# Kernel tuning notes

Measured on AMD Instinct MI355X. Metric: run time of the kernel, lower is better.

Reference implementation:

```python
import jax, jax.numpy as jnp
import numpy as np

DIM = 1024
NUM_HEADS = 16
HEAD_DIM = DIM // NUM_HEADS
SCALE = HEAD_DIM ** -0.5


def setup_inputs() -> dict:
    key = jax.random.key(0)
    k_x, k_qkv, k_pw, k_pb = jax.random.split(key, 4)
    B, S = 2, 2048
    x = jax.random.normal(k_x, (B, S, DIM), dtype=jnp.float32)
    # nn.Linear(dim, 3*dim, bias=False): weight [3*dim, dim]
    w_qkv = jax.random.normal(k_qkv, (3 * DIM, DIM), dtype=jnp.float32) * (DIM ** -0.5)
    # nn.Linear(dim, dim): weight [dim, dim], bias [dim]
    w_proj = jax.random.normal(k_pw, (DIM, DIM), dtype=jnp.float32) * (DIM ** -0.5)
    b_proj = jax.random.normal(k_pb, (DIM,), dtype=jnp.float32) * 0.01
    return {"x": x, "w_qkv": w_qkv, "w_proj": w_proj, "b_proj": b_proj}


def reference(x, w_qkv, w_proj, b_proj):
    B, S, D = x.shape
    qkv = jnp.einsum("bsd,ed->bse", x, w_qkv)  # [B,S,3D]
    q, k, v = jnp.split(qkv, 3, axis=-1)
    def heads(t):  # [B,S,D] -> [B,H,S,hd]
        return t.reshape(B, S, NUM_HEADS, HEAD_DIM).transpose(0, 2, 1, 3)
    q, k, v = heads(q), heads(k), heads(v)
    attn = jnp.einsum("bhqd,bhkd->bhqk", q, k) * SCALE  # [B,H,S,S]
    attn = jax.nn.softmax(attn, axis=-1)
    out = jnp.einsum("bhqk,bhkd->bhqd", attn, v)  # [B,H,S,hd]
    out = out.transpose(0, 2, 1, 3).reshape(B, S, D)
    return jnp.einsum("bsd,ed->bse", out, w_proj) + b_proj
```

## Files before the change

kernel.cpp:

```cpp
#include <hip/hip_runtime.h>
#include <stdint.h>

typedef __bf16 bf16;
typedef __bf16 bf16x8 __attribute__((ext_vector_type(8)));
typedef float f32x4 __attribute__((ext_vector_type(4)));
typedef float f32x16 __attribute__((ext_vector_type(16)));

typedef __attribute__((address_space(1))) void gvoid_t;
typedef __attribute__((address_space(3))) void lvoid_t;

__device__ __forceinline__ void gload16(const void* src, void* lds) {
    __builtin_amdgcn_global_load_lds((gvoid_t*)src, (lvoid_t*)lds, 16, 0, 0);
}

__device__ __forceinline__ float fexp2(float x) {
    float r;
    asm("v_exp_f32 %0, %1" : "=v"(r) : "v"(x));
    return r;
}

__global__ __launch_bounds__(256) void cvt3_kernel(const float* __restrict__ x,
                                                   const float* __restrict__ wqkv,
                                                   const float* __restrict__ wproj,
                                                   bf16* __restrict__ xb,
                                                   bf16* __restrict__ wqkvb,
                                                   bf16* __restrict__ wprojb) {
    int idx = blockIdx.x * 256 + threadIdx.x;
    int stride = gridDim.x * 256;
    for (int i = idx; i < 1048576; i += stride) {
        const float* in;
        bf16* out;
        int j;
        if (i < 524288) { in = x; out = xb; j = i; }
        else if (i < 917504) { in = wqkv; out = wqkvb; j = i - 524288; }
        else { in = wproj; out = wprojb; j = i - 917504; }
        const float4* p = (const float4*)in;
        float4 a = p[(long)j * 2], b = p[(long)j * 2 + 1];
        bf16x8 o;
        o[0] = (bf16)a.x; o[1] = (bf16)a.y; o[2] = (bf16)a.z; o[3] = (bf16)a.w;
        o[4] = (bf16)b.x; o[5] = (bf16)b.y; o[6] = (bf16)b.z; o[7] = (bf16)b.w;
        ((bf16x8*)out)[j] = o;
    }
}

template <bool F32OUT, int BN>
__global__ __launch_bounds__(256) void gemm_bt(const bf16* __restrict__ A,
                                               const bf16* __restrict__ W,
                                               const float* __restrict__ bias,
                                               void* __restrict__ Cout,
                                               const int M, const int N, const int K) {
    constexpr int NT = BN / 32;
    constexpr int BELEMS = BN * 32;
    __shared__ __align__(16) bf16 Alds[3 * 4096];
    __shared__ __align__(16) bf16 Blds[3 * BELEMS];
    const int t = threadIdx.x;
    const int wid = t >> 6, lane = t & 63;
    const int g = lane >> 4, c = lane & 15;
    const int wm = wid >> 1, wn = wid & 1;
    const long bm = (long)blockIdx.y * 128, bn = (long)blockIdx.x * BN;

    f32x4 acc[4][NT] = {};

    const int arow = t >> 2;
    const int acol = (t & 3) * 8;
    const bf16* Asrc = A + (bm + arow) * (long)K + acol;
    const bf16* Bsrc = W + (bn + arow) * (long)K + acol;
    const int dstb = wid * 512;

#define GSTAGE(BI)                                                       \
    {                                                                    \
        bf16* ad = Alds + (BI) * 4096 + dstb;                            \
        bf16* bd = Blds + (BI) * BELEMS + dstb;                          \
        gload16(Asrc, ad);                                               \
        gload16(Asrc + (long)64 * K, ad + 2048);                         \
        gload16(Bsrc, bd);                                               \
        if constexpr (BN == 128) gload16(Bsrc + (long)64 * K, bd + 2048);\
        Asrc += 32;                                                      \
        Bsrc += 32;                                                      \
    }

    auto computeg = [&](int bi) __attribute__((always_inline)) {
        const bf16* Ab = Alds + bi * 4096;
        const bf16* Bb = Blds + bi * BELEMS;
        bf16x8 af[4], bfr[NT];
#pragma unroll
        for (int mt = 0; mt < 4; ++mt)
            af[mt] = *(const bf16x8*)(Ab + (wm * 64 + mt * 16 + c) * 32 + g * 8);
#pragma unroll
        for (int nt = 0; nt < NT; ++nt)
            bfr[nt] = *(const bf16x8*)(Bb + (wn * (BN / 2) + nt * 16 + c) * 32 + g * 8);
#pragma unroll
        for (int mt = 0; mt < 4; ++mt)
#pragma unroll
            for (int nt = 0; nt < NT; ++nt)
                acc[mt][nt] = __builtin_amdgcn_mfma_f32_16x16x32_bf16(af[mt], bfr[nt],
                                                                      acc[mt][nt], 0, 0, 0);
    };

#define GWAITN                                                              \
    if constexpr (BN == 128) { asm volatile("s_waitcnt vmcnt(4)" ::: "memory"); } \
    else { asm volatile("s_waitcnt vmcnt(3)" ::: "memory"); }

#define GSTEP(CUR, NXT)            \
    GWAITN;                        \
    __builtin_amdgcn_s_barrier();  \
    GSTAGE(NXT);                   \
    computeg(CUR);

    GSTAGE(0);
    GSTAGE(1);
    for (int t3 = 0; t3 < 10; ++t3) {
        GSTEP(0, 2)
        GSTEP(1, 0)
        GSTEP(2, 1)
    }
    GWAITN;
    __builtin_amdgcn_s_barrier();
    computeg(0);
    asm volatile("s_waitcnt vmcnt(0)" ::: "memory");
    __builtin_amdgcn_s_barrier();
    computeg(1);
#undef GSTEP
#undef GWAITN
#undef GSTAGE

#pragma unroll
    for (int mt = 0; mt < 4; ++mt) {
#pragma unroll
        for (int nt = 0; nt < NT; ++nt) {
#pragma unroll
            for (int i = 0; i < 4; ++i) {
                const long row = bm + wm * 64 + mt * 16 + g * 4 + i;
                const long col = bn + wn * (BN / 2) + nt * 16 + c;
                if constexpr (F32OUT) {
                    ((float*)Cout)[row * N + col] = acc[mt][nt][i] + bias[col];
                } else {
                    ((bf16*)Cout)[row * N + col] = (bf16)acc[mt][nt][i];
                }
            }
        }
    }
}

__global__ __launch_bounds__(128) void flash_kernel(const bf16* __restrict__ qk,
                                                    const bf16* __restrict__ Vt,
                                                    bf16* __restrict__ attno) {
    __shared__ __align__(16) bf16 KV[24576];
    __shared__ float LP[128];

    const int t = threadIdx.x;
    const int wid = t >> 6, lane = t & 63;
    const int l31 = lane & 31, hl = lane >> 5;

    const int i0 = blockIdx.x;
    const int xcd = i0 & 7, slot = i0 >> 3;
    const int bh = xcd * 4 + (slot >> 4);
    const int qb = slot & 15;
    const int b = bh >> 4, h = bh & 15;
    const int rowbase = b * 2048;
    const int q0w = qb * 128 + wid * 64;

    bf16x8 qfa[4], qfb[4];
    {
        const bf16* qra = qk + (long)(rowbase + q0w + l31) * 2048 + h * 64 + hl * 8;
        const bf16* qrb = qra + 32 * 2048;
        const float qs = 0.18033688f;
#pragma unroll
        for (int ks = 0; ks < 4; ++ks) {
            bf16x8 a = *(const bf16x8*)(qra + ks * 16);
            bf16x8 d = *(const bf16x8*)(qrb + ks * 16);
#pragma unroll
            for (int e = 0; e < 8; ++e) {
                qfa[ks][e] = (bf16)((float)a[e] * qs);
                qfb[ks][e] = (bf16)((float)d[e] * qs);
            }
        }
    }

    const int srow0 = wid * 8 + ((lane >> 3) & 7);
    const int swcol = ((lane & 7) ^ (srow0 & 7)) * 8;
    const bf16* ksn = qk + (long)(rowbase + srow0) * 2048 + 1024 + h * 64 + swcol;
    const bf16* vsn = Vt + (long)(h * 64 + srow0) * 4096 + b * 2048 + swcol;
    const int kchunk = wid * 512;

    int rdoff[4];
#pragma unroll
    for (int ks = 0; ks < 4; ++ks)
        rdoff[ks] = l31 * 64 + (((ks * 2 + hl) ^ (l31 & 7)) * 8);

    float lpA0 = 0.f, lpB0 = 0.f, lpA1 = 0.f, lpB1 = 0.f;
    f32x16 oacc00 = {}, oacc10 = {}, oacc01 = {}, oacc11 = {};

#define STAGE(BI)                                                        \
    {                                                                    \
        bf16* kd = KV + (BI) * 4096 + kchunk;                            \
        bf16* vd = KV + 12288 + (BI) * 4096 + kchunk;                    \
        gload16(ksn, kd);                                                \
        gload16(ksn + 32768, kd + 1024);                                 \
        gload16(ksn + 65536, kd + 2048);                                 \
        gload16(ksn + 98304, kd + 3072);                                 \
        gload16(vsn, vd);                                                \
        gload16(vsn + 65536, vd + 1024);                                 \
        gload16(vsn + 131072, vd + 2048);                                \
        gload16(vsn + 196608, vd + 3072);                                \
        ksn += 131072;                                                   \
        vsn += 64;                                                       \
    }

    auto compute = [&](int bi) __attribute__((always_inline)) {
        const bf16* Kb = KV + bi * 4096;
        const bf16* Vb = KV + 12288 + bi * 4096;
        f32x16 s00 = {}, s10 = {}, s01 = {}, s11 = {};
        __builtin_amdgcn_s_setprio(1);
#pragma unroll
        for (int ks = 0; ks < 4; ++ks) {
            bf16x8 kf0 = *(const bf16x8*)(Kb + rdoff[ks]);
            bf16x8 kf1 = *(const bf16x8*)(Kb + 2048 + rdoff[ks]);
            s00 = __builtin_amdgcn_mfma_f32_32x32x16_bf16(kf0, qfa[ks], s00, 0, 0, 0);
            s10 = __builtin_amdgcn_mfma_f32_32x32x16_bf16(kf1, qfa[ks], s10, 0, 0, 0);
            s01 = __builtin_amdgcn_mfma_f32_32x32x16_bf16(kf0, qfb[ks], s01, 0, 0, 0);
            s11 = __builtin_amdgcn_mfma_f32_32x32x16_bf16(kf1, qfb[ks], s11, 0, 0, 0);
        }
        __builtin_amdgcn_s_setprio(0);
        float p00[16], p10[16], p01[16], p11[16];
#pragma unroll
        for (int r = 0; r < 16; ++r) p00[r] = fexp2(s00[r]);
#pragma unroll
        for (int r = 0; r < 16; ++r) p10[r] = fexp2(s10[r]);
#pragma unroll
        for (int r = 0; r < 16; ++r) p01[r] = fexp2(s01[r]);
#pragma unroll
        for (int r = 0; r < 16; ++r) p11[r] = fexp2(s11[r]);
#pragma unroll
        for (int r = 0; r < 8; ++r) {
            lpA0 += p00[r] + p10[r];
            lpB0 += p00[r + 8] + p10[r + 8];
            lpA1 += p01[r] + p11[r];
            lpB1 += p01[r + 8] + p11[r + 8];
        }
        __builtin_amdgcn_s_setprio(1);
#pragma unroll
        for (int ks = 0; ks < 4; ++ks) {
            bf16x8 vf0 = *(const bf16x8*)(Vb + rdoff[ks]);
            bf16x8 vf1 = *(const bf16x8*)(Vb + 2048 + rdoff[ks]);
            const int s = (ks & 1) * 8;
            {
                const float* pp = (ks < 2) ? p00 : p10;
                unsigned wA, wB, wC, wD;
                asm("v_cvt_pk_bf16_f32 %0, %1, %2" : "=v"(wA) : "v"(pp[s + 0]), "v"(pp[s + 1]));
                asm("v_cvt_pk_bf16_f32 %0, %1, %2" : "=v"(wB) : "v"(pp[s + 4]), "v"(pp[s + 5]));
                asm("v_cvt_pk_bf16_f32 %0, %1, %2" : "=v"(wC) : "v"(pp[s + 2]), "v"(pp[s + 3]));
                asm("v_cvt_pk_bf16_f32 %0, %1, %2" : "=v"(wD) : "v"(pp[s + 6]), "v"(pp[s + 7]));
                asm("v_permlane32_swap_b32 %0, %1" : "+v"(wA), "+v"(wB));
                asm("v_permlane32_swap_b32 %0, %1" : "+v"(wC), "+v"(wD));
                union { unsigned w[4]; bf16x8 v; } pu;
                pu.w[0] = wA; pu.w[1] = wC; pu.w[2] = wB; pu.w[3] = wD;
                oacc00 = __builtin_amdgcn_mfma_f32_32x32x16_bf16(pu.v, vf0, oacc00, 0, 0, 0);
                oacc10 = __builtin_amdgcn_mfma_f32_32x32x16_bf16(pu.v, vf1, oacc10, 0, 0, 0);
            }
            {
                const float* pp = (ks < 2) ? p01 : p11;
                unsigned wA, wB, wC, wD;
                asm("v_cvt_pk_bf16_f32 %0, %1, %2" : "=v"(wA) : "v"(pp[s + 0]), "v"(pp[s + 1]));
                asm("v_cvt_pk_bf16_f32 %0, %1, %2" : "=v"(wB) : "v"(pp[s + 4]), "v"(pp[s + 5]));
                asm("v_cvt_pk_bf16_f32 %0, %1, %2" : "=v"(wC) : "v"(pp[s + 2]), "v"(pp[s + 3]));
                asm("v_cvt_pk_bf16_f32 %0, %1, %2" : "=v"(wD) : "v"(pp[s + 6]), "v"(pp[s + 7]));
                asm("v_permlane32_swap_b32 %0, %1" : "+v"(wA), "+v"(wB));
                asm("v_permlane32_swap_b32 %0, %1" : "+v"(wC), "+v"(wD));
                union { unsigned w[4]; bf16x8 v; } pu;
                pu.w[0] = wA; pu.w[1] = wC; pu.w[2] = wB; pu.w[3] = wD;
                oacc01 = __builtin_amdgcn_mfma_f32_32x32x16_bf16(pu.v, vf0, oacc01, 0, 0, 0);
                oacc11 = __builtin_amdgcn_mfma_f32_32x32x16_bf16(pu.v, vf1, oacc11, 0, 0, 0);
            }
        }
        __builtin_amdgcn_s_setprio(0);
    };

    STAGE(0);
    STAGE(1);

#define FSTEP(CUR, NXT)                                    \
    asm volatile("s_waitcnt vmcnt(8)" ::: "memory");       \
    __builtin_amdgcn_s_barrier();                          \
    STAGE(NXT);                                            \
    compute(CUR);

    for (int t3 = 0; t3 < 10; ++t3) {
        FSTEP(0, 2)
        FSTEP(1, 0)
        FSTEP(2, 1)
    }
    asm volatile("s_waitcnt vmcnt(8)" ::: "memory");
    __builtin_amdgcn_s_barrier();
    compute(0);
    asm volatile("s_waitcnt vmcnt(0)" ::: "memory");
    __builtin_amdgcn_s_barrier();
    compute(1);
#undef FSTEP
#undef STAGE

    float lp0 = lpA0 + lpB0;
    float lp1 = lpA1 + lpB1;
    lp0 += __shfl_xor(lp0, 32);
    lp1 += __shfl_xor(lp1, 32);
    if (lane < 32) {
        LP[wid * 64 + l31] = lp0;
        LP[wid * 64 + 32 + l31] = lp1;
    }
    __builtin_amdgcn_s_barrier();

#pragma unroll
    for (int r = 0; r < 16; ++r) {
        const int qrow = (r & 3) + 8 * (r >> 2) + 4 * hl;
        const float i0v = 1.0f / LP[wid * 64 + qrow];
        const float i1v = 1.0f / LP[wid * 64 + 32 + qrow];
        const long rb0 = (long)(rowbase + q0w + qrow) * 1024 + h * 64 + l31;
        const long rb1 = (long)(rowbase + q0w + 32 + qrow) * 1024 + h * 64 + l31;
        attno[rb0] = (bf16)(oacc00[r] * i0v);
        attno[rb0 + 32] = (bf16)(oacc10[r] * i0v);
        attno[rb1] = (bf16)(oacc01[r] * i1v);
        attno[rb1 + 32] = (bf16)(oacc11[r] * i1v);
    }
}

extern "C" void kernel_launch(void* const* d_in, const int* in_sizes, int n_in,
                              void* d_out, int out_size, void* d_ws, size_t ws_size,
                              hipStream_t stream) {
    const float* x = (const float*)d_in[0];
    const float* wqkv = (const float*)d_in[1];
    const float* wproj = (const float*)d_in[2];
    const float* bproj = (const float*)d_in[3];

    char* ws = (char*)d_ws;
    bf16* xb     = (bf16*)(ws);
    bf16* wqkvb  = (bf16*)(ws + 8388608);
    bf16* wprojb = (bf16*)(ws + 14680064);
    bf16* qk     = (bf16*)(ws + 16777216);
    bf16* Vt     = (bf16*)(ws + 33554432);
    bf16* attno  = (bf16*)(ws + 41943040);
    if (ws_size < 50331648) return;

    cvt3_kernel<<<2048, 256, 0, stream>>>(x, wqkv, wproj, xb, wqkvb, wprojb);

    gemm_bt<false, 128><<<dim3(16, 32), 256, 0, stream>>>(xb, wqkvb, nullptr, qk,
                                                          4096, 2048, 1024);

    gemm_bt<false, 128><<<dim3(32, 8), 256, 0, stream>>>(wqkvb + 2048 * 1024, xb, nullptr, Vt,
                                                         1024, 4096, 1024);

    flash_kernel<<<512, 128, 0, stream>>>(qk, Vt, attno);

    gemm_bt<true, 128><<<dim3(8, 32), 256, 0, stream>>>(attno, wprojb, bproj, d_out,
                                                        4096, 1024, 1024);
}
```

Measured before the change: 133.7 us.

## Split flash attention over two KV halves and add combine kernel

The attention kernel now splits each (batch, head, query-block) over two halves of the key sequence, doubling the grid so more blocks occupy the CUs. Each half writes unnormalized bf16 partial outputs and row sums into workspace buffers that alias dead inputs. A new combine kernel adds the halves and divides by the summed denominators. The V-projection and output-projection GEMMs also switch to a smaller N tile so they launch more blocks. This adds an extra memory pass and an extra bf16 rounding of the partials.

```diff
diff --git a/kernel.cpp b/kernel.cpp
--- a/kernel.cpp
+++ b/kernel.cpp
@@ -144,9 +144,10 @@
 
 __global__ __launch_bounds__(128) void flash_kernel(const bf16* __restrict__ qk,
                                                     const bf16* __restrict__ Vt,
-                                                    bf16* __restrict__ attno) {
+                                                    bf16* __restrict__ P0,
+                                                    bf16* __restrict__ P1,
+                                                    float* __restrict__ lpar) {
     __shared__ __align__(16) bf16 KV[24576];
-    __shared__ float LP[128];
 
     const int t = threadIdx.x;
     const int wid = t >> 6, lane = t & 63;
@@ -154,8 +155,9 @@
 
     const int i0 = blockIdx.x;
     const int xcd = i0 & 7, slot = i0 >> 3;
-    const int bh = xcd * 4 + (slot >> 4);
-    const int qb = slot & 15;
+    const int bh = xcd * 4 + (slot >> 5);
+    const int rem = slot & 31;
+    const int qb = rem >> 1, kvh = rem & 1;
     const int b = bh >> 4, h = bh & 15;
     const int rowbase = b * 2048;
     const int q0w = qb * 128 + wid * 64;
@@ -179,8 +181,8 @@
 
     const int srow0 = wid * 8 + ((lane >> 3) & 7);
     const int swcol = ((lane & 7) ^ (srow0 & 7)) * 8;
-    const bf16* ksn = qk + (long)(rowbase + srow0) * 2048 + 1024 + h * 64 + swcol;
-    const bf16* vsn = Vt + (long)(h * 64 + srow0) * 4096 + b * 2048 + swcol;
+    const bf16* ksn = qk + (long)(rowbase + kvh * 1024 + srow0) * 2048 + 1024 + h * 64 + swcol;
+    const bf16* vsn = Vt + (long)(h * 64 + srow0) * 4096 + b * 2048 + kvh * 1024 + swcol;
     const int kchunk = wid * 512;
 
     int rdoff[4];
@@ -285,17 +287,19 @@
     STAGE(NXT);                                            \
     compute(CUR);
 
-    for (int t3 = 0; t3 < 10; ++t3) {
+    for (int t3 = 0; t3 < 4; ++t3) {
         FSTEP(0, 2)
         FSTEP(1, 0)
         FSTEP(2, 1)
     }
+    FSTEP(0, 2)
+    FSTEP(1, 0)
     asm volatile("s_waitcnt vmcnt(8)" ::: "memory");
     __builtin_amdgcn_s_barrier();
-    compute(0);
+    compute(2);
     asm volatile("s_waitcnt vmcnt(0)" ::: "memory");
     __builtin_amdgcn_s_barrier();
-    compute(1);
+    compute(0);
 #undef FSTEP
 #undef STAGE
 
@@ -304,22 +308,42 @@
     lp0 += __shfl_xor(lp0, 32);
     lp1 += __shfl_xor(lp1, 32);
     if (lane < 32) {
-        LP[wid * 64 + l31] = lp0;
-        LP[wid * 64 + 32 + l31] = lp1;
-    }
-    __builtin_amdgcn_s_barrier();
-
+        const int qloc = qb * 128 + wid * 64 + l31;
+        float* lp = lpar + kvh * 65536 + bh * 2048 + qloc;
+        lp[0] = lp0;
+        lp[32] = lp1;
+    }
+
+    bf16* Pd = kvh ? P1 : P0;
 #pragma unroll
     for (int r = 0; r < 16; ++r) {
         const int qrow = (r & 3) + 8 * (r >> 2) + 4 * hl;
-        const float i0v = 1.0f / LP[wid * 64 + qrow];
-        const float i1v = 1.0f / LP[wid * 64 + 32 + qrow];
         const long rb0 = (long)(rowbase + q0w + qrow) * 1024 + h * 64 + l31;
         const long rb1 = (long)(rowbase + q0w + 32 + qrow) * 1024 + h * 64 + l31;
-        attno[rb0] = (bf16)(oacc00[r] * i0v);
-        attno[rb0 + 32] = (bf16)(oacc10[r] * i0v);
-        attno[rb1] = (bf16)(oacc01[r] * i1v);
-        attno[rb1 + 32] = (bf16)(oacc11[r] * i1v);
+        Pd[rb0] = (bf16)oacc00[r];
+        Pd[rb0 + 32] = (bf16)oacc10[r];
+        Pd[rb1] = (bf16)oacc01[r];
+        Pd[rb1 + 32] = (bf16)oacc11[r];
+    }
+}
+
+__global__ __launch_bounds__(256) void combine_kernel(bf16* __restrict__ P0,
+                                                      const bf16* __restrict__ P1,
+                                                      const float* __restrict__ lpar) {
+    int idx = blockIdx.x * 256 + threadIdx.x;
+    int stride = gridDim.x * 256;
+    for (int gi = idx; gi < 524288; gi += stride) {
+        const int e0 = gi * 8;
+        const int row = e0 >> 10, col = e0 & 1023;
+        const int li = ((row >> 11) * 16 + (col >> 6)) * 2048 + (row & 2047);
+        const float inv = 1.0f / (lpar[li] + lpar[li + 65536]);
+        bf16x8 a = ((const bf16x8*)P0)[gi];
+        bf16x8 b8 = ((const bf16x8*)P1)[gi];
+        bf16x8 o;
+#pragma unroll
+        for (int e = 0; e < 8; ++e)
+            o[e] = (bf16)(((float)a[e] + (float)b8[e]) * inv);
+        ((bf16x8*)P0)[gi] = o;
     }
 }
 
@@ -333,7 +357,9 @@
 
     char* ws = (char*)d_ws;
     bf16* xb     = (bf16*)(ws);
+    bf16* P1     = (bf16*)(ws);
     bf16* wqkvb  = (bf16*)(ws + 8388608);
+    float* lpar  = (float*)(ws + 8388608);
     bf16* wprojb = (bf16*)(ws + 14680064);
     bf16* qk     = (bf16*)(ws + 16777216);
     bf16* Vt     = (bf16*)(ws + 33554432);
@@ -345,11 +371,13 @@
     gemm_bt<false, 128><<<dim3(16, 32), 256, 0, stream>>>(xb, wqkvb, nullptr, qk,
                                                           4096, 2048, 1024);
 
-    gemm_bt<false, 128><<<dim3(32, 8), 256, 0, stream>>>(wqkvb + 2048 * 1024, xb, nullptr, Vt,
-                                                         1024, 4096, 1024);
-
-    flash_kernel<<<512, 128, 0, stream>>>(qk, Vt, attno);
-
-    gemm_bt<true, 128><<<dim3(8, 32), 256, 0, stream>>>(attno, wprojb, bproj, d_out,
+    gemm_bt<false, 64><<<dim3(64, 8), 256, 0, stream>>>(wqkvb + 2048 * 1024, xb, nullptr, Vt,
+                                                        1024, 4096, 1024);
+
+    flash_kernel<<<1024, 128, 0, stream>>>(qk, Vt, attno, P1, lpar);
+
+    combine_kernel<<<1024, 256, 0, stream>>>(attno, P1, lpar);
+
+    gemm_bt<true, 64><<<dim3(16, 32), 256, 0, stream>>>(attno, wprojb, bproj, d_out,
                                                         4096, 1024, 1024);
 }
```

Result: no change. 131.5 us (-1.6%).
